# Kernel optimization log

Measured on AMD Instinct MI355X. Metric: run time of the kernel, lower is better.

The kernel has to match this reference:

```python
import jax, jax.numpy as jnp
import numpy as np

K = 3        # kernel_size
S = 1        # stride
PAD = 1      # padding
BITS = 8
MAX_VAL = 2.5
DELTA = MAX_VAL / (2 ** (BITS - 1) - 1)


def im2col(x, k, s, p):
    # x: [N, C, H, W] -> cols: [N, C*k*k, h_out*w_out] (same layout as F.unfold)
    n, c, h, w = x.shape
    h_out = (h - k + 2 * p) // s + 1
    w_out = (w - k + 2 * p) // s + 1
    xp = jnp.pad(x, ((0, 0), (0, 0), (p, p), (p, p)))
    patches = jnp.stack(
        [xp[:, :, i : i + (h_out - 1) * s + 1 : s, j : j + (w_out - 1) * s + 1 : s]
         for i in range(k) for j in range(k)],
        axis=2,
    )  # [N, C, k*k, h_out, w_out]
    return patches.reshape(n, c * k * k, h_out * w_out), h_out, w_out


def setup_inputs() -> dict:
    key = jax.random.key(0)
    k1, k2 = jax.random.split(key)
    x = jax.random.normal(k1, (8, 64, 32, 32), dtype=jnp.float32)
    W = jax.random.normal(k2, (64, 64, 3, 3), dtype=jnp.float32)  # adder parameter
    return {"x": x, "W": W}


def reference(x, W):
    # Inference path: needs_input_grad[0] is False, so weights are NOT quantized.
    n = x.shape[0]
    n_filters = W.shape[0]
    cols, h_out, w_out = im2col(x, K, S, PAD)              # [N, CKK, L]
    X_col = jnp.transpose(cols, (1, 2, 0)).reshape(cols.shape[1], -1)  # [CKK, L*N]
    W_col = W.reshape(n_filters, -1)                        # [F, CKK]
    # Stream over filters to avoid the [F, CKK, P] broadcast blowup.
    out = jax.lax.map(lambda w: -jnp.abs(w[:, None] - X_col).sum(0), W_col)  # [F, P]
    out = out.reshape(n_filters, h_out, w_out, n)
    return jnp.transpose(out, (3, 0, 1, 2))  # [N, F, h_out, w_out]
```

## Files before the change

### kernel.cpp

```cpp
#include <hip/hip_runtime.h>
#include <stdint.h>


typedef _Float16 half2v __attribute__((ext_vector_type(2)));

#define XS   20
#define RH   18
#define CH2  32
#define XCHW (RH * XS)
#define W2_ELEMS (CH2 * 16 * 4 * 9)
#define WS_NEEDED (W2_ELEMS * 4 + 64 * 4)

__global__ __launch_bounds__(64)
void prep_kernel(const float* __restrict__ W, uint32_t* __restrict__ W2,
                 float* __restrict__ SW) {
    const int f    = blockIdx.x;
    const int lane = threadIdx.x;
    float s = 0.0f;
    for (int i = lane; i < CH2 * 9; i += 64) {
        const int ch2 = i / 9;
        const int k   = i - ch2 * 9;
        const float a = W[(size_t)f * 576 + (2 * ch2) * 9 + k];
        const float b = W[(size_t)f * 576 + (2 * ch2 + 1) * 9 + k];
        const _Float16 ha = (_Float16)a;
        const _Float16 hb = (_Float16)b;
        uint16_t ua = __builtin_bit_cast(uint16_t, ha);
        uint16_t ub = __builtin_bit_cast(uint16_t, hb);
        W2[((size_t)ch2 * 16 + (f >> 2)) * 36 + (f & 3) * 9 + k] =
            (uint32_t)ua | ((uint32_t)ub << 16);
        s += (float)ha + (float)hb;
    }
#pragma unroll
    for (int m = 32; m >= 1; m >>= 1) s += __shfl_xor(s, m, 64);
    if (lane == 0) SW[f] = s;
}

__global__ __launch_bounds__(512)
void adder2d_kernel(const float* __restrict__ x,
                    const uint32_t* __restrict__ W2,
                    const float* __restrict__ SW,
                    float* __restrict__ out) {
    __shared__ uint32_t xs[CH2 * XCHW];

    const int bid     = blockIdx.x;
    const int quarter = bid & 3;
    const int fg      = (bid >> 2) & 15;
    const int n       = bid >> 6;
    const int r0      = (quarter >> 1) * 16;
    const int c0      = (quarter & 1) * 16;
    const int tid     = threadIdx.x;

    {
        const int ch2s = tid >> 4;
        const int sub  = tid & 15;
        const float* xa = x + ((size_t)n * 64 + 2 * ch2s) * 1024;
        for (int cell = sub; cell < RH * RH; cell += 16) {
            const int row = cell / RH;
            const int col = cell - row * RH;
            const int ir  = r0 + row - 1;
            const int ic  = c0 + col - 1;
            float a = 0.0f, b = 0.0f;
            if ((unsigned)ir < 32u && (unsigned)ic < 32u) {
                a = xa[ir * 32 + ic];
                b = xa[1024 + ir * 32 + ic];
            }
            const _Float16 ha = (_Float16)a;
            const _Float16 hb = (_Float16)b;
            xs[ch2s * XCHW + row * XS + col] =
                (uint32_t)__builtin_bit_cast(uint16_t, ha) |
                ((uint32_t)__builtin_bit_cast(uint16_t, hb) << 16);
        }
    }
    __syncthreads();

    const int wave = __builtin_amdgcn_readfirstlane(tid >> 6);
    const int lane = tid & 63;
    const int tx   = lane & 7;
    const int ty   = lane >> 3;

    const half2v one2 = {(_Float16)1.0f, (_Float16)1.0f};
    float acc[16];
    float sx[4];
#pragma unroll
    for (int i = 0; i < 16; ++i) acc[i] = 0.0f;
#pragma unroll
    for (int i = 0; i < 4; ++i) sx[i] = 0.0f;

#pragma unroll
    for (int i = 0; i < 4; ++i) {
        const int ch2 = wave * 4 + i;
        const uint32_t* wp = W2 + ((size_t)ch2 * 16 + fg) * 36;

        uint32_t xw[4][4];
#pragma unroll
        for (int r = 0; r < 4; ++r) {
            const uint32_t* p = &xs[ch2 * XCHW + (2 * ty + r) * XS + 2 * tx];
            const uint2 A = *(const uint2*)p;
            const uint2 B = *(const uint2*)(p + 2);
            xw[r][0] = A.x; xw[r][1] = A.y; xw[r][2] = B.x; xw[r][3] = B.y;
        }

#pragma unroll
        for (int f = 0; f < 4; ++f) {
#pragma unroll
            for (int k = 0; k < 9; ++k) {
                const int ki = k / 3, kj = k - 3 * ki;
                const half2v w2 = __builtin_bit_cast(half2v, wp[f * 9 + k]);
#pragma unroll
                for (int sr = 0; sr < 2; ++sr)
#pragma unroll
                    for (int sc = 0; sc < 2; ++sc) {
                        const half2v xv =
                            __builtin_bit_cast(half2v, xw[sr + ki][sc + kj]);
                        const half2v m = __builtin_elementwise_min(w2, xv);
                        acc[f * 4 + sr * 2 + sc] = __builtin_amdgcn_fdot2(
                            m, one2, acc[f * 4 + sr * 2 + sc], false);
                    }
            }
        }
#pragma unroll
        for (int k = 0; k < 9; ++k) {
            const int ki = k / 3, kj = k - 3 * ki;
#pragma unroll
            for (int sr = 0; sr < 2; ++sr)
#pragma unroll
                for (int sc = 0; sc < 2; ++sc) {
                    const half2v xv =
                        __builtin_bit_cast(half2v, xw[sr + ki][sc + kj]);
                    sx[sr * 2 + sc] = __builtin_amdgcn_fdot2(
                        xv, one2, sx[sr * 2 + sc], false);
                }
        }
    }

    __syncthreads();
    float* ps = (float*)xs;
#pragma unroll
    for (int s = 0; s < 16; ++s) ps[((wave * 64 + lane) * 20) + s] = acc[s];
#pragma unroll
    for (int s = 0; s < 4; ++s) ps[((wave * 64 + lane) * 20) + 16 + s] = sx[s];
    __syncthreads();

    const int px  = tid & 255;
    const int fp  = tid >> 8;
    const int row = px >> 4, col = px & 15;
    const int lane_s = (row >> 1) * 8 + (col >> 1);
    const int sub_s  = (row & 1) * 2 + (col & 1);

    float sxs = 0.0f;
#pragma unroll
    for (int w = 0; w < 8; ++w)
        sxs += ps[(w * 64 + lane_s) * 20 + 16 + sub_s];
#pragma unroll
    for (int f2 = 0; f2 < 2; ++f2) {
        const int f = fp * 2 + f2;
        float m = 0.0f;
#pragma unroll
        for (int w = 0; w < 8; ++w)
            m += ps[(w * 64 + lane_s) * 20 + f * 4 + sub_s];
        const float val = 2.0f * m - SW[fg * 4 + f] - sxs;
        out[(((size_t)n * 64 + fg * 4 + f) * 32 + r0 + row) * 32 + c0 + col] = val;
    }
}

#define FB_CCHUNK 16
#define FB_XROW 36
#define FB_XCH (10 * FB_XROW)
#define FB_WPAD 12
__global__ __launch_bounds__(256, 6)
void adder2d_fb(const float* __restrict__ x, const float* __restrict__ Wt,
                float* __restrict__ out) {
    __shared__ float fxs[FB_CCHUNK * FB_XCH];
    __shared__ float fws[4 * FB_CCHUNK * FB_WPAD];
    const int bid = blockIdx.x;
    const int ks = bid & 3, fg = (bid >> 2) & 15, tile = (bid >> 6) & 3, n = bid >> 8;
    const int c0 = ks * FB_CCHUNK, f0 = fg * 4, i0 = tile * 8, tid = threadIdx.x;
    for (int idx = tid; idx < 4 * FB_CCHUNK * 9; idx += 256) {
        const int f = idx / (FB_CCHUNK * 9), rem = idx - f * (FB_CCHUNK * 9);
        const int cc = rem / 9, kk = rem - cc * 9;
        fws[(f * FB_CCHUNK + cc) * FB_WPAD + kk] =
            Wt[((size_t)(f0 + f) * 64 + (c0 + cc)) * 9 + kk];
    }
    const float* xn = x + ((size_t)n * 64 + c0) * 1024;
    for (int idx = tid; idx < FB_CCHUNK * FB_XCH; idx += 256) {
        const int cc = idx / FB_XCH, rem = idx - cc * FB_XCH;
        const int row = rem / FB_XROW, col = rem - row * FB_XROW;
        const int ir = i0 + row - 1, ic = col - 1;
        float v = 0.0f;
        if ((unsigned)ir < 32u && (unsigned)ic < 32u) v = xn[cc * 1024 + ir * 32 + ic];
        fxs[idx] = v;
    }
    __syncthreads();
    const int r = tid >> 5, j = tid & 31;
    float acc[4] = {0, 0, 0, 0};
#pragma unroll 2
    for (int cc = 0; cc < FB_CCHUNK; ++cc) {
        const float* xp = &fxs[cc * FB_XCH + r * FB_XROW + j];
        const float x00 = xp[0], x01 = xp[1], x02 = xp[2];
        const float x10 = xp[36], x11 = xp[37], x12 = xp[38];
        const float x20 = xp[72], x21 = xp[73], x22 = xp[74];
#pragma unroll
        for (int f = 0; f < 4; ++f) {
            const float* wq = &fws[(f * FB_CCHUNK + cc) * FB_WPAD];
            acc[f] += fabsf(wq[0] - x00) + fabsf(wq[1] - x01) + fabsf(wq[2] - x02)
                    + fabsf(wq[3] - x10) + fabsf(wq[4] - x11) + fabsf(wq[5] - x12)
                    + fabsf(wq[6] - x20) + fabsf(wq[7] - x21) + fabsf(wq[8] - x22);
        }
    }
    const int irow = i0 + r;
#pragma unroll
    for (int f = 0; f < 4; ++f)
        atomicAdd(&out[(((size_t)n * 64 + (f0 + f)) * 32 + irow) * 32 + j], -acc[f]);
}

extern "C" void kernel_launch(void* const* d_in, const int* in_sizes, int n_in,
                              void* d_out, int out_size, void* d_ws, size_t ws_size,
                              hipStream_t stream) {
    const float* x  = (const float*)d_in[0];
    const float* W  = (const float*)d_in[1];
    float* out      = (float*)d_out;

    if (ws_size >= (size_t)WS_NEEDED) {
        uint32_t* W2 = (uint32_t*)d_ws;
        float* SW    = (float*)((char*)d_ws + W2_ELEMS * 4);
        hipLaunchKernelGGL(prep_kernel, dim3(64), dim3(64), 0, stream, W, W2, SW);
        hipLaunchKernelGGL(adder2d_kernel, dim3(512), dim3(512), 0, stream,
                           x, W2, SW, out);
    } else {
        hipMemsetAsync(d_out, 0, (size_t)out_size * sizeof(float), stream);
        hipLaunchKernelGGL(adder2d_fb, dim3(2048), dim3(256), 0, stream, x, W, out);
    }
}
```

Baseline: 79.45 us.

## Interleave filter weights for vector loads and stage them in shared memory

New measurement: 80.55 us. About the same (+1.4%).

```diff
diff --git a/kernel.cpp b/kernel.cpp
--- a/kernel.cpp
+++ b/kernel.cpp
@@ -8,8 +8,8 @@
 #define RH   18
 #define CH2  32
 #define XCHW (RH * XS)
-#define W2_ELEMS (CH2 * 16 * 4 * 9)
-#define WS_NEEDED (W2_ELEMS * 4 + 64 * 4)
+#define W2_U32 (CH2 * 16 * 9 * 4)
+#define WS_NEEDED (W2_U32 * 4 + 64 * 4)
 
 __global__ __launch_bounds__(64)
 void prep_kernel(const float* __restrict__ W, uint32_t* __restrict__ W2,
@@ -24,9 +24,9 @@
         const float b = W[(size_t)f * 576 + (2 * ch2 + 1) * 9 + k];
         const _Float16 ha = (_Float16)a;
         const _Float16 hb = (_Float16)b;
-        uint16_t ua = __builtin_bit_cast(uint16_t, ha);
-        uint16_t ub = __builtin_bit_cast(uint16_t, hb);
-        W2[((size_t)ch2 * 16 + (f >> 2)) * 36 + (f & 3) * 9 + k] =
+        const uint16_t ua = __builtin_bit_cast(uint16_t, ha);
+        const uint16_t ub = __builtin_bit_cast(uint16_t, hb);
+        W2[((((size_t)ch2 * 16 + (f >> 2)) * 9 + k) << 2) + (f & 3)] =
             (uint32_t)ua | ((uint32_t)ub << 16);
         s += (float)ha + (float)hb;
     }
@@ -35,12 +35,13 @@
     if (lane == 0) SW[f] = s;
 }
 
-__global__ __launch_bounds__(512)
+__global__ __launch_bounds__(512, 2)
 void adder2d_kernel(const float* __restrict__ x,
-                    const uint32_t* __restrict__ W2,
+                    const uint4* __restrict__ W2,
                     const float* __restrict__ SW,
                     float* __restrict__ out) {
     __shared__ uint32_t xs[CH2 * XCHW];
+    __shared__ uint4 wl[CH2 * 9];
 
     const int bid     = blockIdx.x;
     const int quarter = bid & 3;
@@ -49,6 +50,12 @@
     const int r0      = (quarter >> 1) * 16;
     const int c0      = (quarter & 1) * 16;
     const int tid     = threadIdx.x;
+
+    for (int idx = tid; idx < CH2 * 9; idx += 512) {
+        const int ch2 = idx / 9;
+        const int k   = idx - 9 * ch2;
+        wl[idx] = W2[((size_t)ch2 * 16 + fg) * 9 + k];
+    }
 
     {
         const int ch2s = tid >> 4;
@@ -89,7 +96,6 @@
 #pragma unroll
     for (int i = 0; i < 4; ++i) {
         const int ch2 = wave * 4 + i;
-        const uint32_t* wp = W2 + ((size_t)ch2 * 16 + fg) * 36;
 
         uint32_t xw[4][4];
 #pragma unroll
@@ -101,34 +107,25 @@
         }
 
 #pragma unroll
-        for (int f = 0; f < 4; ++f) {
-#pragma unroll
-            for (int k = 0; k < 9; ++k) {
-                const int ki = k / 3, kj = k - 3 * ki;
-                const half2v w2 = __builtin_bit_cast(half2v, wp[f * 9 + k]);
-#pragma unroll
-                for (int sr = 0; sr < 2; ++sr)
-#pragma unroll
-                    for (int sc = 0; sc < 2; ++sc) {
-                        const half2v xv =
-                            __builtin_bit_cast(half2v, xw[sr + ki][sc + kj]);
-                        const half2v m = __builtin_elementwise_min(w2, xv);
-                        acc[f * 4 + sr * 2 + sc] = __builtin_amdgcn_fdot2(
-                            m, one2, acc[f * 4 + sr * 2 + sc], false);
-                    }
-            }
-        }
-#pragma unroll
         for (int k = 0; k < 9; ++k) {
             const int ki = k / 3, kj = k - 3 * ki;
+            const uint4 wk = wl[ch2 * 9 + k];
+            const uint32_t wf_[4] = {wk.x, wk.y, wk.z, wk.w};
 #pragma unroll
             for (int sr = 0; sr < 2; ++sr)
 #pragma unroll
                 for (int sc = 0; sc < 2; ++sc) {
                     const half2v xv =
                         __builtin_bit_cast(half2v, xw[sr + ki][sc + kj]);
-                    sx[sr * 2 + sc] = __builtin_amdgcn_fdot2(
-                        xv, one2, sx[sr * 2 + sc], false);
+                    const int sub = sr * 2 + sc;
+                    sx[sub] = __builtin_amdgcn_fdot2(xv, one2, sx[sub], false);
+#pragma unroll
+                    for (int f = 0; f < 4; ++f) {
+                        const half2v w2 = __builtin_bit_cast(half2v, wf_[f]);
+                        const half2v m  = __builtin_elementwise_min(w2, xv);
+                        acc[f * 4 + sub] =
+                            __builtin_amdgcn_fdot2(m, one2, acc[f * 4 + sub], false);
+                    }
                 }
         }
     }
@@ -222,10 +219,10 @@
 
     if (ws_size >= (size_t)WS_NEEDED) {
         uint32_t* W2 = (uint32_t*)d_ws;
-        float* SW    = (float*)((char*)d_ws + W2_ELEMS * 4);
+        float* SW    = (float*)((char*)d_ws + (size_t)W2_U32 * 4);
         hipLaunchKernelGGL(prep_kernel, dim3(64), dim3(64), 0, stream, W, W2, SW);
         hipLaunchKernelGGL(adder2d_kernel, dim3(512), dim3(512), 0, stream,
-                           x, W2, SW, out);
+                           x, (const uint4*)W2, SW, out);
     } else {
         hipMemsetAsync(d_out, 0, (size_t)out_size * sizeof(float), stream);
         hipLaunchKernelGGL(adder2d_fb, dim3(2048), dim3(256), 0, stream, x, W, out);
```
